# Optimization experiments

Hardware: AMD Instinct MI355X
Metric: run time of the kernel (lower is better)

Reference implementation:

```python
import jax, jax.numpy as jnp
import numpy as np

H = 256; NH = 8; DH = H // NH; L = 2; B = 32; S = 512; FIN = 199; A = 4


def _ln(x, g, b):
    m = jnp.mean(x, -1, keepdims=True)
    v = jnp.mean((x - m) ** 2, -1, keepdims=True)
    return (x - m) / jnp.sqrt(v + 1e-5) * g + b


def _grn(x, fc1w, fc1b, fc2w, fc2b, gw, gb, ggw, ggb, lg, lb):
    # GatedResidualNetwork, input_dim == output_dim so no skip layer, no context
    h = jax.nn.elu(x @ fc1w + fc1b)
    h = jax.nn.elu(h @ fc2w + fc2b)
    g = (h @ gw + gb) * jax.nn.sigmoid(h @ ggw + ggb)  # GLU
    return _ln(g + x, lg, lb)


def _attn(h, wq, bq, wk, bk, wv, bv, wo, bo):
    b, s, _ = h.shape
    q = (h @ wq + bq).reshape(b, s, NH, DH)
    k = (h @ wk + bk).reshape(b, s, NH, DH)
    v = (h @ wv + bv).reshape(b, s, NH, DH)
    scores = jnp.einsum('bqhd,bkhd->bhqk', q, k) / jnp.sqrt(jnp.float32(DH))
    mask = jnp.triu(jnp.ones((s, s), dtype=bool), 1)  # causal: mask strictly-future
    scores = jnp.where(mask, -jnp.inf, scores)
    aw = jax.nn.softmax(scores, axis=-1)
    ctx = jnp.einsum('bhqk,bkhd->bqhd', aw, v).reshape(b, s, H)
    return ctx @ wo + bo, aw


def _pe(s, d):
    pos = jnp.arange(s, dtype=jnp.float32)[:, None]
    div = jnp.exp(jnp.arange(0, d, 2, dtype=jnp.float32) * (-jnp.log(10000.0) / d))
    pe = jnp.zeros((s, d), dtype=jnp.float32)
    pe = pe.at[:, 0::2].set(jnp.sin(pos * div)).at[:, 1::2].set(jnp.cos(pos * div))
    return pe


def setup_inputs():
    key = jax.random.key(0)
    ks = iter(jax.random.split(key, 80))
    def nrm(shape, sc=0.02):
        return (jax.random.normal(next(ks), shape) * sc).astype(jnp.float32)
    d = {}
    d['x'] = jax.random.normal(next(ks), (B, S, FIN), dtype=jnp.float32)
    d['time_features'] = jax.random.normal(next(ks), (B, S, 3), dtype=jnp.float32)
    d['fp_w'] = nrm((FIN, H)); d['fp_b'] = jnp.zeros((H,), jnp.float32)
    d['tp_w'] = nrm((3, H));   d['tp_b'] = jnp.zeros((H,), jnp.float32)
    d['ip_w'] = nrm((H, H));   d['ip_b'] = jnp.zeros((H,), jnp.float32)
    for nm in ['wq', 'wk', 'wv', 'wo']:
        d[nm] = nrm((L, H, H))
    for nm in ['bq', 'bk', 'bv', 'bo']:
        d[nm] = jnp.zeros((L, H), jnp.float32)
    d['ln_g'] = jnp.ones((L, H), jnp.float32); d['ln_b'] = jnp.zeros((L, H), jnp.float32)
    for nm in ['g_fc1w', 'g_fc2w', 'g_gw', 'g_ggw']:
        d[nm] = nrm((L, H, H))
    for nm in ['g_fc1b', 'g_fc2b', 'g_gb', 'g_ggb']:
        d[nm] = jnp.zeros((L, H), jnp.float32)
    d['g_lg'] = jnp.ones((L, H), jnp.float32); d['g_lb'] = jnp.zeros((L, H), jnp.float32)
    for nm in ['f_fc1w', 'f_fc2w', 'f_gw', 'f_ggw']:
        d[nm] = nrm((H, H))
    for nm in ['f_fc1b', 'f_fc2b', 'f_gb', 'f_ggb']:
        d[nm] = jnp.zeros((H,), jnp.float32)
    d['f_lg'] = jnp.ones((H,), jnp.float32); d['f_lb'] = jnp.zeros((H,), jnp.float32)
    d['out_w'] = nrm((H, A)); d['out_b'] = jnp.zeros((A,), jnp.float32)
    return d


def reference(x, time_features, fp_w, fp_b, tp_w, tp_b, ip_w, ip_b,
              wq, bq, wk, bk, wv, bv, wo, bo, ln_g, ln_b,
              g_fc1w, g_fc1b, g_fc2w, g_fc2b, g_gw, g_gb, g_ggw, g_ggb, g_lg, g_lb,
              f_fc1w, f_fc1b, f_fc2w, f_fc2b, f_gw, f_gb, f_ggw, f_ggb, f_lg, f_lb,
              out_w, out_b):
    s = x.shape[1]
    hidden = (x @ fp_w + fp_b) + (time_features @ tp_w + tp_b)
    hidden = hidden @ ip_w + ip_b
    hidden = hidden + _pe(s, H)[None]
    aw = None
    for i in range(L):
        ao, aw = _attn(hidden, wq[i], bq[i], wk[i], bk[i], wv[i], bv[i], wo[i], bo[i])
        hidden = _ln(hidden + ao, ln_g[i], ln_b[i])
        hidden = _grn(hidden, g_fc1w[i], g_fc1b[i], g_fc2w[i], g_fc2b[i],
                      g_gw[i], g_gb[i], g_ggw[i], g_ggb[i], g_lg[i], g_lb[i])
    hidden = _grn(hidden, f_fc1w, f_fc1b, f_fc2w, f_fc2b, f_gw, f_gb, f_ggw, f_ggb, f_lg, f_lb)
    final = hidden[:, -1, :]
    logits = final @ out_w + out_b  # [B, A], one column per target asset
    return (logits, aw)
```

## Files before the change

kernel.cpp:

```cpp
#include <hip/hip_runtime.h>
#include <math.h>
#include <cstddef>

#define H 256
#define NH 8
#define DH 32
#define LAYERS 2
#define BB 32
#define SS 512
#define FINDIM 199
#define AA 4
#define T_TOK (BB*SS)
#define KIN 224

typedef unsigned short u16;
typedef unsigned int u32;
typedef __attribute__((ext_vector_type(8))) short short8;
typedef __attribute__((ext_vector_type(4))) float f4;

__device__ __forceinline__ float b2f(u16 v){
  unsigned u = ((unsigned)v) << 16;
  return __builtin_bit_cast(float, u);
}
__device__ __forceinline__ u16 f2b(float f){
  unsigned u = __builtin_bit_cast(unsigned, f);
  unsigned r = (u + 0x7fffu + ((u >> 16) & 1u)) >> 16;
  return (u16)r;
}
__device__ __forceinline__ float wave_sum(float v){
  #pragma unroll
  for (int mk=1; mk<64; mk<<=1) v += __shfl_xor(v, mk, 64);
  return v;
}

#define GLD_LDS16(g, l) \
  __builtin_amdgcn_global_load_lds((const __attribute__((address_space(1))) void*)(g), \
                                   (__attribute__((address_space(3))) void*)(l), 16, 0, 0)

template<int KC, int WK>
__device__ __forceinline__ void stage_acc(
    const u16* Xl, int sx, const u16* __restrict__ Wt,
    int c0, int l16, int lq, f4 acc[2][2])
{
  #pragma unroll
  for (int mi=0;mi<2;mi++)
    #pragma unroll
    for (int ni=0;ni<2;ni++) acc[mi][ni] = (f4){0.f,0.f,0.f,0.f};
  #pragma unroll
  for (int kc=0;kc<KC;kc++){
    short8 af[2], bf[2];
    af[0] = *(const short8*)&Xl[(l16)*sx      + kc*32 + lq*8];
    af[1] = *(const short8*)&Xl[(16+l16)*sx   + kc*32 + lq*8];
    bf[0] = *(const short8*)(Wt + (size_t)(c0+l16)*WK    + kc*32 + lq*8);
    bf[1] = *(const short8*)(Wt + (size_t)(c0+16+l16)*WK + kc*32 + lq*8);
    #pragma unroll
    for (int mi=0;mi<2;mi++)
      #pragma unroll
      for (int ni=0;ni<2;ni++)
        acc[mi][ni] = __builtin_amdgcn_mfma_f32_16x16x32_bf16(af[mi], bf[ni], acc[mi][ni], 0,0,0);
  }
}

template<int DO_ELU>
__device__ __forceinline__ void stage_store(
    f4 acc[2][2], const float* __restrict__ bias,
    int c0, int l16, int lq, u16* Yl, int sy)
{
  #pragma unroll
  for (int ni=0;ni<2;ni++){
    int col = c0 + ni*16 + l16;
    float bc = bias[col];
    #pragma unroll
    for (int mi=0;mi<2;mi++){
      #pragma unroll
      for (int r=0;r<4;r++){
        int row = mi*16 + lq*4 + r;
        float v = acc[mi][ni][r] + bc;
        if (DO_ELU) v = v > 0.f ? v : expm1f(v);
        Yl[row*sy + col] = f2b(v);
      }
    }
  }
}

__device__ __forceinline__ void tile_load256(const u16* g, u16* Yl, int sy, int t){
  #pragma unroll
  for (int j=0;j<2;j++){
    int u = t + j*512;
    int row = u >> 5, cu = u & 31;
    *(short8*)&Yl[row*sy + cu*8] = *(const short8*)(g + (size_t)row*H + cu*8);
  }
}

__device__ __forceinline__ void tile_ln(
    const u16* Yl, int sy, const float* __restrict__ g, const float* __restrict__ b,
    u16* out, int t)
{
  int w = t >> 6, lane = t & 63;
  #pragma unroll
  for (int rr=0;rr<4;rr++){
    int row = w*4 + rr;
    float xv[4];
    #pragma unroll
    for (int j=0;j<4;j++) xv[j] = b2f(Yl[row*sy + lane*4 + j]);
    float s=0.f, ss=0.f;
    #pragma unroll
    for (int j=0;j<4;j++){ s += xv[j]; ss += xv[j]*xv[j]; }
    s = wave_sum(s); ss = wave_sum(ss);
    float mean = s * (1.0f/H);
    float var  = ss * (1.0f/H) - mean*mean;
    float rstd = rsqrtf(var + 1e-5f);
    ushort4 o;
    int col = lane*4;
    o.x = f2b((xv[0]-mean)*rstd*g[col+0] + b[col+0]);
    o.y = f2b((xv[1]-mean)*rstd*g[col+1] + b[col+1]);
    o.z = f2b((xv[2]-mean)*rstd*g[col+2] + b[col+2]);
    o.w = f2b((xv[3]-mean)*rstd*g[col+3] + b[col+3]);
    *(ushort4*)(out + (size_t)row*H + col) = o;
  }
}

struct WPtrs { const float* p[21]; };

__global__ __launch_bounds__(256) void wconv_kernel(WPtrs wp, u16* __restrict__ dst){
  __shared__ float tl[64][65];
  int mb = blockIdx.x >> 4, tile = blockIdx.x & 15;
  int k0 = (tile >> 2) * 64, n0 = (tile & 3) * 64;
  const float* src = wp.p[mb];
  int t = threadIdx.x;
  int r = t >> 4, cg = t & 15;
  #pragma unroll
  for (int p4=0;p4<4;p4++){
    f4 v = *(const f4*)(src + (size_t)(k0 + r + p4*16)*H + n0 + cg*4);
    tl[r+p4*16][cg*4+0]=v[0]; tl[r+p4*16][cg*4+1]=v[1];
    tl[r+p4*16][cg*4+2]=v[2]; tl[r+p4*16][cg*4+3]=v[3];
  }
  __syncthreads();
  u16* db = dst + (size_t)mb*H*H;
  #pragma unroll
  for (int p4=0;p4<4;p4++){
    int rn = r + p4*16;
    ushort4 o;
    o.x = f2b(tl[cg*4+0][rn]); o.y = f2b(tl[cg*4+1][rn]);
    o.z = f2b(tl[cg*4+2][rn]); o.w = f2b(tl[cg*4+3][rn]);
    *(ushort4*)(db + (size_t)(n0+rn)*H + k0 + cg*4) = o;
  }
}

__global__ __launch_bounds__(256) void wcat_kernel(
    const float* __restrict__ fp_w, const float* __restrict__ tp_w,
    u16* __restrict__ wcat){
  int idx = blockIdx.x*256 + threadIdx.x;
  if (idx >= 256*KIN) return;
  int n = idx / KIN, k2 = idx % KIN;
  float v = 0.f;
  if (k2 < FINDIM) v = fp_w[(size_t)k2*H + n];
  else if (k2 < FINDIM+3) v = tp_w[(size_t)(k2-FINDIM)*H + n];
  wcat[idx] = f2b(v);
}

__global__ __launch_bounds__(256) void xconv_kernel(
    const float* __restrict__ x, const float* __restrict__ tf,
    u16* __restrict__ ab){
  size_t idx = (size_t)blockIdx.x*256 + threadIdx.x;
  if (idx >= (size_t)T_TOK*KIN) return;
  int tok = idx / KIN, k2 = idx % KIN;
  float v = 0.f;
  if (k2 < FINDIM) v = x[(size_t)tok*FINDIM + k2];
  else if (k2 < FINDIM+3) v = tf[(size_t)tok*3 + (k2-FINDIM)];
  ab[idx] = f2b(v);
}

#define SA (KIN+8)
#define SY (H+8)

__global__ __launch_bounds__(512) void input_kernel(
    const u16* __restrict__ ab, const u16* __restrict__ wcat,
    const float* __restrict__ fp_b, const float* __restrict__ tp_b,
    const u16* __restrict__ ipw, const float* __restrict__ ip_b,
    u16* __restrict__ hid){
  __shared__ u16 Al[32*SA];
  __shared__ u16 Tl[32*SY];
  int t = threadIdx.x;
  int tok0 = blockIdx.x * 32;
  int lane = t & 63, w = t >> 6;
  int l16 = lane & 15, lq = lane >> 4;
  int c0 = w * 32;

  #pragma unroll
  for (int j=0;j<2;j++){
    int u = t + j*512;
    if (u < 896){
      int row = u / 28, cu = u % 28;
      *(short8*)&Al[row*SA + cu*8] = *(const short8*)(ab + (size_t)(tok0+row)*KIN + cu*8);
    }
  }
  __syncthreads();

  f4 acc[2][2];
  stage_acc<7, KIN>(Al, SA, wcat, c0, l16, lq, acc);
  #pragma unroll
  for (int ni=0;ni<2;ni++){
    int col = c0 + ni*16 + l16;
    float bc = fp_b[col] + tp_b[col];
    #pragma unroll
    for (int mi=0;mi<2;mi++)
      #pragma unroll
      for (int r=0;r<4;r++){
        int row = mi*16 + lq*4 + r;
        Tl[row*SY + col] = f2b(acc[mi][ni][r] + bc);
      }
  }
  __syncthreads();

  stage_acc<8, H>(Tl, SY, ipw, c0, l16, lq, acc);
  #pragma unroll
  for (int ni=0;ni<2;ni++){
    int col = c0 + ni*16 + l16;
    float bc = ip_b[col];
    int ii = col >> 1;
    float div = __expf((float)(2*ii) * -0.03597789207803197f);
    #pragma unroll
    for (int mi=0;mi<2;mi++)
      #pragma unroll
      for (int r=0;r<4;r++){
        int row = mi*16 + lq*4 + r;
        int s = (tok0 + row) & (SS-1);
        float arg = (float)s * div;
        float pe = (col & 1) ? cosf(arg) : sinf(arg);
        hid[(size_t)(tok0+row)*H + col] = f2b(acc[mi][ni][r] + bc + pe);
      }
  }
}

__global__ __launch_bounds__(512) void oproj_ln_kernel(
    const u16* __restrict__ ctx, u16* __restrict__ hid,
    const u16* __restrict__ wo, const float* __restrict__ bo,
    const float* __restrict__ g, const float* __restrict__ b){
  __shared__ u16 Xl[32*SY];
  __shared__ u16 Rl[32*SY];
  int t = threadIdx.x;
  int tok0 = blockIdx.x * 32;
  int lane = t & 63, w = t >> 6;
  int l16 = lane & 15, lq = lane >> 4;
  int c0 = w * 32;
  u16* hb = hid + (size_t)tok0*H;

  tile_load256(ctx + (size_t)tok0*H, Xl, SY, t);
  tile_load256(hb, Rl, SY, t);
  __syncthreads();

  f4 acc[2][2];
  stage_acc<8, H>(Xl, SY, wo, c0, l16, lq, acc);
  __syncthreads();
  #pragma unroll
  for (int ni=0;ni<2;ni++){
    int col = c0 + ni*16 + l16;
    float bc = bo[col];
    #pragma unroll
    for (int mi=0;mi<2;mi++)
      #pragma unroll
      for (int r=0;r<4;r++){
        int row = mi*16 + lq*4 + r;
        float y = acc[mi][ni][r] + bc + b2f(Rl[row*SY + col]);
        Xl[row*SY + col] = f2b(y);
      }
  }
  __syncthreads();
  tile_ln(Xl, SY, g, b, hb, t);
}

__global__ __launch_bounds__(512) void grn_kernel(
    u16* __restrict__ hid,
    const u16* __restrict__ fc1, const u16* __restrict__ fc2,
    const u16* __restrict__ gw,  const u16* __restrict__ ggw,
    const float* __restrict__ b1, const float* __restrict__ b2,
    const float* __restrict__ gb, const float* __restrict__ ggb,
    const float* __restrict__ lg, const float* __restrict__ lb){
  __shared__ u16 Xl[32*SY];
  __shared__ u16 H1[32*SY];
  __shared__ u16 H2[32*SY];
  int t = threadIdx.x;
  int tok0 = blockIdx.x * 32;
  int lane = t & 63, w = t >> 6;
  int l16 = lane & 15, lq = lane >> 4;
  int c0 = w * 32;
  u16* hb = hid + (size_t)tok0*H;

  tile_load256(hb, Xl, SY, t);
  __syncthreads();

  f4 acc[2][2];
  stage_acc<8, H>(Xl, SY, fc1, c0, l16, lq, acc);
  stage_store<1>(acc, b1, c0, l16, lq, H1, SY);
  __syncthreads();
  stage_acc<8, H>(H1, SY, fc2, c0, l16, lq, acc);
  stage_store<1>(acc, b2, c0, l16, lq, H2, SY);
  __syncthreads();
  stage_acc<8, H>(H2, SY, gw, c0, l16, lq, acc);
  stage_store<0>(acc, gb, c0, l16, lq, H1, SY);
  __syncthreads();
  stage_acc<8, H>(H2, SY, ggw, c0, l16, lq, acc);
  __syncthreads();
  #pragma unroll
  for (int ni=0;ni<2;ni++){
    int col = c0 + ni*16 + l16;
    float bc = ggb[col];
    #pragma unroll
    for (int mi=0;mi<2;mi++)
      #pragma unroll
      for (int r=0;r<4;r++){
        int row = mi*16 + lq*4 + r;
        float gg = acc[mi][ni][r] + bc;
        float sg = 1.0f/(1.0f + __expf(-gg));
        float y  = b2f(H1[row*SY + col]) * sg + b2f(Xl[row*SY + col]);
        H2[row*SY + col] = f2b(y);
      }
  }
  __syncthreads();
  tile_ln(H2, SY, lg, lb, hb, t);
}

struct GemmJob  { const u16* Wt; const float* bias; u16* C; };
struct GemmBatch{ GemmJob j[3]; };

__global__ __launch_bounds__(256) void gemm_bf16(
    const u16* __restrict__ A, GemmBatch jb) {
  __shared__ u16 smem[128*64 + 64*64];
  u16* As  = smem;
  u16* Wsm = smem + 128*64;
  const GemmJob job = jb.j[blockIdx.z];
  const u16* Wt = job.Wt;
  int t = threadIdx.x;
  int m0 = blockIdx.x * 128;
  int n0 = blockIdx.y * 64;
  int lane = t & 63, w = t >> 6;
  int wr = (w >> 1) * 64;
  int wc = (w & 1) * 32;
  int l16 = lane & 15, lq = lane >> 4;

  f4 acc[4][2];
  #pragma unroll
  for (int mi=0;mi<4;mi++)
    #pragma unroll
    for (int ni=0;ni<2;ni++) acc[mi][ni] = (f4){0.f,0.f,0.f,0.f};

  for (int k0=0;k0<256;k0+=64){
    #pragma unroll
    for (int ja=0;ja<4;ja++){
      int ub = (w*4 + ja)*64;
      int u  = ub + lane;
      int m  = u >> 3, c = u & 7, kx = c ^ (m & 7);
      const u16* g = A + (size_t)(m0+m)*H + k0 + kx*8;
      GLD_LDS16(g, As + (size_t)ub*8);
    }
    #pragma unroll
    for (int jb2=0;jb2<2;jb2++){
      int ub = (w*2 + jb2)*64;
      int u  = ub + lane;
      int n  = u >> 3, c = u & 7, kx = c ^ (n & 7);
      const u16* g = Wt + (size_t)(n0+n)*H + k0 + kx*8;
      GLD_LDS16(g, Wsm + (size_t)ub*8);
    }
    __syncthreads();
    #pragma unroll
    for (int kc=0;kc<2;kc++){
      short8 af[4], bf[2];
      int kx = kc*4 + lq;
      #pragma unroll
      for (int mi=0;mi<4;mi++){
        int m = wr + mi*16 + l16;
        int un = (m<<3) | (kx ^ (m&7));
        af[mi] = *(short8*)&As[un*8];
      }
      #pragma unroll
      for (int ni=0;ni<2;ni++){
        int n = wc + ni*16 + l16;
        int un = (n<<3) | (kx ^ (n&7));
        bf[ni] = *(short8*)&Wsm[un*8];
      }
      #pragma unroll
      for (int mi=0;mi<4;mi++)
        #pragma unroll
        for (int ni=0;ni<2;ni++)
          acc[mi][ni] = __builtin_amdgcn_mfma_f32_16x16x32_bf16(af[mi], bf[ni], acc[mi][ni], 0,0,0);
    }
    __syncthreads();
  }

  u16* Cl = smem;
  #pragma unroll
  for (int ni=0;ni<2;ni++){
    int coll = wc + ni*16 + l16;
    float bcol = job.bias[n0 + coll];
    #pragma unroll
    for (int mi=0;mi<4;mi++){
      #pragma unroll
      for (int r=0;r<4;r++){
        int rowl = wr + mi*16 + lq*4 + r;
        Cl[rowl*68 + coll] = f2b(acc[mi][ni][r] + bcol);
      }
    }
  }
  __syncthreads();
  #pragma unroll
  for (int q2=0;q2<4;q2++){
    int u = q2*256 + t;
    int row = u >> 3, cu = u & 7;
    short8 val = *(short8*)&Cl[row*68 + cu*8];
    *(short8*)(job.C + (size_t)(m0+row)*H + n0 + cu*8) = val;
  }
}

template<int WRITE_AW>
__global__ __launch_bounds__(256) void attn_kernel(
    const u16* __restrict__ q, const u16* __restrict__ k,
    const u16* __restrict__ v, float* __restrict__ aw,
    u16* __restrict__ ctx) {
  __shared__ u16 Vt[DH][SS+8];
  __shared__ u16 Plds[4][16][72];
  int t  = threadIdx.x;
  int zg = blockIdx.x;
  int bh = blockIdx.y;
  int b  = bh >> 3, h = bh & 7;
  int lane = t & 63, w = t >> 6;
  int l16 = lane & 15, lq = lane >> 4;
  const float scale = 0.17677669529663687f;

  #pragma unroll
  for (int rep=0;rep<2;rep++){
    int kk = t + rep*256;
    const u16* vp = v + ((size_t)(b*SS + kk))*H + h*DH;
    short8 r0 = *(const short8*)(vp);
    short8 r1 = *(const short8*)(vp+8);
    short8 r2 = *(const short8*)(vp+16);
    short8 r3 = *(const short8*)(vp+24);
    #pragma unroll
    for (int j=0;j<8;j++){
      Vt[j][kk]    = (u16)r0[j];
      Vt[8+j][kk]  = (u16)r1[j];
      Vt[16+j][kk] = (u16)r2[j];
      Vt[24+j][kk] = (u16)r3[j];
    }
  }
  __syncthreads();

  for (int it=0; it<4; it++){
    int qt  = zg + it*2;
    int qr0 = qt*64 + w*16;
    int KT  = qt*4 + w + 1;
    short8 af = *(const short8*)(q + ((size_t)(b*SS + qr0 + l16))*H + h*DH + lq*8);

    float l[4] = {0.f,0.f,0.f,0.f};
    f4 o[2] = {(f4){0.f,0.f,0.f,0.f}, (f4){0.f,0.f,0.f,0.f}};
    u32 pk0[32], pk1[32];

    #pragma unroll
    for (int c8=0;c8<8;c8++){
      if (c8*4 < KT){
        #pragma unroll
        for (int j=0;j<4;j++){
          int kt = c8*4 + j;
          float p[4] = {0.f,0.f,0.f,0.f};
          if (kt < KT){
            short8 bfr = *(const short8*)(k + ((size_t)(b*SS + kt*16 + l16))*H + h*DH + lq*8);
            f4 cc = (f4){0.f,0.f,0.f,0.f};
            cc = __builtin_amdgcn_mfma_f32_16x16x32_bf16(af, bfr, cc, 0,0,0);
            int col = kt*16 + l16;
            #pragma unroll
            for (int i=0;i<4;i++){
              int qi = qr0 + lq*4 + i;
              float sc = (col <= qi) ? cc[i]*scale : -3.0e38f;
              p[i] = __expf(sc);
              l[i] += p[i];
            }
          }
          u16 pb[4];
          #pragma unroll
          for (int i=0;i<4;i++) pb[i] = f2b(p[i]);
          if (WRITE_AW){
            pk0[kt] = (u32)pb[0] | ((u32)pb[1] << 16);
            pk1[kt] = (u32)pb[2] | ((u32)pb[3] << 16);
          }
          #pragma unroll
          for (int i=0;i<4;i++) Plds[w][lq*4+i][j*16+l16] = pb[i];
        }
        #pragma unroll
        for (int kc=0;kc<2;kc++){
          short8 pa = *(short8*)&Plds[w][l16][kc*32 + lq*8];
          #pragma unroll
          for (int dt=0;dt<2;dt++){
            short8 vb = *(const short8*)&Vt[dt*16 + l16][c8*64 + kc*32 + lq*8];
            o[dt] = __builtin_amdgcn_mfma_f32_16x16x32_bf16(pa, vb, o[dt], 0,0,0);
          }
        }
      }
    }

    #pragma unroll
    for (int i=0;i<4;i++){
      #pragma unroll
      for (int mk=1; mk<16; mk<<=1) l[i] += __shfl_xor(l[i], mk, 64);
    }
    float inv[4];
    #pragma unroll
    for (int i=0;i<4;i++) inv[i] = 1.0f / l[i];

    if (WRITE_AW){
      float* ab = aw + (size_t)bh*SS*SS;
      #pragma unroll
      for (int kt=0;kt<32;kt++){
        if (kt < KT){
          int col = kt*16 + l16;
          float pv[4] = { b2f((u16)pk0[kt]), b2f((u16)(pk0[kt]>>16)),
                          b2f((u16)pk1[kt]), b2f((u16)(pk1[kt]>>16)) };
          #pragma unroll
          for (int i=0;i<4;i++){
            int qi = qr0 + lq*4 + i;
            ab[(size_t)qi*SS + col] = (col <= qi) ? pv[i]*inv[i] : 0.f;
          }
        }
      }
      int c4base = KT*4;
      f4 z = (f4){0.f,0.f,0.f,0.f};
      #pragma unroll
      for (int ri=0;ri<4;ri++){
        int row = qr0 + ri*4 + lq;
        for (int j=l16; j < 128 - c4base; j += 16)
          *(f4*)&ab[(size_t)row*SS + (size_t)(c4base+j)*4] = z;
      }
    }

    #pragma unroll
    for (int dt=0;dt<2;dt++){
      #pragma unroll
      for (int i=0;i<4;i++){
        int row = qr0 + lq*4 + i;
        ctx[((size_t)(b*SS + row))*H + h*DH + dt*16 + l16] = f2b(o[dt][i]*inv[i]);
      }
    }
  }
}

__global__ __launch_bounds__(128) void logits_kernel(
    const u16* __restrict__ hid, const float* __restrict__ ow,
    const float* __restrict__ ob, float* __restrict__ out){
  int t = threadIdx.x;
  int b = t >> 2, a = t & 3;
  const u16* hr = hid + ((size_t)b*SS + (SS-1))*H;
  float acc = ob[a];
  for (int k2=0;k2<H;k2++) acc = fmaf(b2f(hr[k2]), ow[k2*AA + a], acc);
  out[t] = acc;
}

extern "C" void kernel_launch(void* const* d_in, const int* in_sizes, int n_in,
                              void* d_out, int out_size, void* d_ws, size_t ws_size,
                              hipStream_t stream){
  (void)in_sizes; (void)n_in; (void)out_size; (void)ws_size;
  const float* x      = (const float*)d_in[0];
  const float* tf     = (const float*)d_in[1];
  const float* fp_w   = (const float*)d_in[2];
  const float* fp_b   = (const float*)d_in[3];
  const float* tp_w   = (const float*)d_in[4];
  const float* tp_b   = (const float*)d_in[5];
  const float* ip_w   = (const float*)d_in[6];
  const float* ip_b   = (const float*)d_in[7];
  const float* wq     = (const float*)d_in[8];
  const float* wk     = (const float*)d_in[9];
  const float* wv     = (const float*)d_in[10];
  const float* wo     = (const float*)d_in[11];
  const float* bq     = (const float*)d_in[12];
  const float* bk     = (const float*)d_in[13];
  const float* bv     = (const float*)d_in[14];
  const float* bo     = (const float*)d_in[15];
  const float* ln_g   = (const float*)d_in[16];
  const float* ln_b   = (const float*)d_in[17];
  const float* g_fc1w = (const float*)d_in[18];
  const float* g_fc2w = (const float*)d_in[19];
  const float* g_gw   = (const float*)d_in[20];
  const float* g_ggw  = (const float*)d_in[21];
  const float* g_fc1b = (const float*)d_in[22];
  const float* g_fc2b = (const float*)d_in[23];
  const float* g_gb   = (const float*)d_in[24];
  const float* g_ggb  = (const float*)d_in[25];
  const float* g_lg   = (const float*)d_in[26];
  const float* g_lb   = (const float*)d_in[27];
  const float* f_fc1w = (const float*)d_in[28];
  const float* f_fc2w = (const float*)d_in[29];
  const float* f_gw   = (const float*)d_in[30];
  const float* f_ggw  = (const float*)d_in[31];
  const float* f_fc1b = (const float*)d_in[32];
  const float* f_fc2b = (const float*)d_in[33];
  const float* f_gb   = (const float*)d_in[34];
  const float* f_ggb  = (const float*)d_in[35];
  const float* f_lg   = (const float*)d_in[36];
  const float* f_lb   = (const float*)d_in[37];
  const float* out_w  = (const float*)d_in[38];
  const float* out_b  = (const float*)d_in[39];

  float* logits = (float*)d_out;
  float* aw     = logits + BB*AA;

  u16* wts = (u16*)d_ws;
  const size_t WMAT = (size_t)H*H;
  u16* wcat = wts  + 21*WMAT;
  u16* abuf = wcat + (size_t)H*KIN;
  u16* hid  = abuf + (size_t)T_TOK*KIN;
  size_t BUF = (size_t)T_TOK * H;
  u16* buf1 = hid  + BUF;
  u16* buf2 = buf1 + BUF;
  u16* buf3 = buf2 + BUF;

  WPtrs wp;
  wp.p[0]  = ip_w;
  wp.p[1]  = wq;        wp.p[2]  = wq + WMAT;
  wp.p[3]  = wk;        wp.p[4]  = wk + WMAT;
  wp.p[5]  = wv;        wp.p[6]  = wv + WMAT;
  wp.p[7]  = wo;        wp.p[8]  = wo + WMAT;
  wp.p[9]  = g_fc1w;    wp.p[10] = g_fc1w + WMAT;
  wp.p[11] = g_fc2w;    wp.p[12] = g_fc2w + WMAT;
  wp.p[13] = g_gw;      wp.p[14] = g_gw + WMAT;
  wp.p[15] = g_ggw;     wp.p[16] = g_ggw + WMAT;
  wp.p[17] = f_fc1w;    wp.p[18] = f_fc2w;
  wp.p[19] = f_gw;      wp.p[20] = f_ggw;
  const int WT_IP=0, WT_Q=1, WT_K=3, WT_V=5, WT_O=7,
            WT_FC1=9, WT_FC2=11, WT_GW=13, WT_GGW=15,
            WT_FFC1=17, WT_FFC2=18, WT_FGW=19, WT_FGGW=20;

  dim3 b256(256), b512(512);
  dim3 gAttn(2, BB*NH);
  dim3 gTok(T_TOK/32);

  wconv_kernel<<<21*16, b256, 0, stream>>>(wp, wts);
  wcat_kernel<<<(H*KIN+255)/256, b256, 0, stream>>>(fp_w, tp_w, wcat);
  xconv_kernel<<<(T_TOK*KIN+255)/256, b256, 0, stream>>>(x, tf, abuf);
  input_kernel<<<gTok, b512, 0, stream>>>(abuf, wcat, fp_b, tp_b,
                                          wts + (size_t)WT_IP*WMAT, ip_b, hid);

  for (int i=0;i<LAYERS;i++){
    const size_t BOFF = (size_t)i*H;
    GemmBatch gb;
    gb.j[0] = { wts + (size_t)(WT_Q+i)*WMAT, bq+BOFF, buf1 };
    gb.j[1] = { wts + (size_t)(WT_K+i)*WMAT, bk+BOFF, buf2 };
    gb.j[2] = { wts + (size_t)(WT_V+i)*WMAT, bv+BOFF, buf3 };
    gemm_bf16<<<dim3(T_TOK/128, H/64, 3), b256, 0, stream>>>(hid, gb);
    if (i == LAYERS-1)
      attn_kernel<1><<<gAttn, b256, 0, stream>>>(buf1, buf2, buf3, aw, buf1);
    else
      attn_kernel<0><<<gAttn, b256, 0, stream>>>(buf1, buf2, buf3, aw, buf1);
    oproj_ln_kernel<<<gTok, b512, 0, stream>>>(buf1, hid,
        wts + (size_t)(WT_O+i)*WMAT, bo+BOFF, ln_g+BOFF, ln_b+BOFF);
    grn_kernel<<<gTok, b512, 0, stream>>>(hid,
        wts + (size_t)(WT_FC1+i)*WMAT, wts + (size_t)(WT_FC2+i)*WMAT,
        wts + (size_t)(WT_GW+i)*WMAT,  wts + (size_t)(WT_GGW+i)*WMAT,
        g_fc1b+BOFF, g_fc2b+BOFF, g_gb+BOFF, g_ggb+BOFF,
        g_lg+BOFF, g_lb+BOFF);
  }

  grn_kernel<<<gTok, b512, 0, stream>>>(hid,
      wts + (size_t)WT_FFC1*WMAT, wts + (size_t)WT_FFC2*WMAT,
      wts + (size_t)WT_FGW*WMAT,  wts + (size_t)WT_FGGW*WMAT,
      f_fc1b, f_fc2b, f_gb, f_ggb, f_lg, f_lb);

  logits_kernel<<<1, 128, 0, stream>>>(hid, out_w, out_b, logits);
}
```

Baseline: 673.6 us.

## Fuse prep kernels, fuse oproj+LN with GRN, coalesce attention-weight stores

Merges the three weight/input conversion kernels into one prep launch. Fuses the output-projection+LayerNorm kernel with the following GRN kernel so the normalized hidden tile stays in LDS instead of round-tripping through global memory. Rewrites the attention-weight write to stage probabilities in LDS and emit float4 row-coalesced stores, and swaps expm1f/sinf/cosf for fast intrinsics. Also adds occupancy hints to launch bounds; fast intrinsics may slightly reduce accuracy, and the new Plds buffer declaration is not visible here.

```diff
diff --git a/kernel.cpp b/kernel.cpp
--- a/kernel.cpp
+++ b/kernel.cpp
@@ -37,6 +37,9 @@
   __builtin_amdgcn_global_load_lds((const __attribute__((address_space(1))) void*)(g), \
                                    (__attribute__((address_space(3))) void*)(l), 16, 0, 0)
 
+#define SA (KIN+8)
+#define SY (H+8)
+
 template<int KC, int WK>
 __device__ __forceinline__ void stage_acc(
     const u16* Xl, int sx, const u16* __restrict__ Wt,
@@ -76,7 +79,7 @@
       for (int r=0;r<4;r++){
         int row = mi*16 + lq*4 + r;
         float v = acc[mi][ni][r] + bc;
-        if (DO_ELU) v = v > 0.f ? v : expm1f(v);
+        if (DO_ELU) v = v > 0.f ? v : (__expf(v) - 1.0f);
         Yl[row*sy + col] = f2b(v);
       }
     }
@@ -92,9 +95,10 @@
   }
 }
 
+template<int TO_LDS>
 __device__ __forceinline__ void tile_ln(
     const u16* Yl, int sy, const float* __restrict__ g, const float* __restrict__ b,
-    u16* out, int t)
+    u16* dst, int t)
 {
   int w = t >> 6, lane = t & 63;
   #pragma unroll
@@ -116,65 +120,61 @@
     o.y = f2b((xv[1]-mean)*rstd*g[col+1] + b[col+1]);
     o.z = f2b((xv[2]-mean)*rstd*g[col+2] + b[col+2]);
     o.w = f2b((xv[3]-mean)*rstd*g[col+3] + b[col+3]);
-    *(ushort4*)(out + (size_t)row*H + col) = o;
+    if (TO_LDS) *(ushort4*)(dst + (size_t)row*SY + col) = o;
+    else        *(ushort4*)(dst + (size_t)row*H  + col) = o;
   }
 }
 
 struct WPtrs { const float* p[21]; };
 
-__global__ __launch_bounds__(256) void wconv_kernel(WPtrs wp, u16* __restrict__ dst){
-  __shared__ float tl[64][65];
-  int mb = blockIdx.x >> 4, tile = blockIdx.x & 15;
-  int k0 = (tile >> 2) * 64, n0 = (tile & 3) * 64;
-  const float* src = wp.p[mb];
+__global__ __launch_bounds__(256) void prep_kernel(
+    WPtrs wp, u16* __restrict__ wts,
+    const float* __restrict__ fp_w, const float* __restrict__ tp_w,
+    u16* __restrict__ wcat,
+    const float* __restrict__ x, const float* __restrict__ tf,
+    u16* __restrict__ abuf){
+  int bid = blockIdx.x;
   int t = threadIdx.x;
-  int r = t >> 4, cg = t & 15;
-  #pragma unroll
-  for (int p4=0;p4<4;p4++){
-    f4 v = *(const f4*)(src + (size_t)(k0 + r + p4*16)*H + n0 + cg*4);
-    tl[r+p4*16][cg*4+0]=v[0]; tl[r+p4*16][cg*4+1]=v[1];
-    tl[r+p4*16][cg*4+2]=v[2]; tl[r+p4*16][cg*4+3]=v[3];
-  }
-  __syncthreads();
-  u16* db = dst + (size_t)mb*H*H;
-  #pragma unroll
-  for (int p4=0;p4<4;p4++){
-    int rn = r + p4*16;
-    ushort4 o;
-    o.x = f2b(tl[cg*4+0][rn]); o.y = f2b(tl[cg*4+1][rn]);
-    o.z = f2b(tl[cg*4+2][rn]); o.w = f2b(tl[cg*4+3][rn]);
-    *(ushort4*)(db + (size_t)(n0+rn)*H + k0 + cg*4) = o;
-  }
-}
-
-__global__ __launch_bounds__(256) void wcat_kernel(
-    const float* __restrict__ fp_w, const float* __restrict__ tp_w,
-    u16* __restrict__ wcat){
-  int idx = blockIdx.x*256 + threadIdx.x;
-  if (idx >= 256*KIN) return;
-  int n = idx / KIN, k2 = idx % KIN;
-  float v = 0.f;
-  if (k2 < FINDIM) v = fp_w[(size_t)k2*H + n];
-  else if (k2 < FINDIM+3) v = tp_w[(size_t)(k2-FINDIM)*H + n];
-  wcat[idx] = f2b(v);
-}
-
-__global__ __launch_bounds__(256) void xconv_kernel(
-    const float* __restrict__ x, const float* __restrict__ tf,
-    u16* __restrict__ ab){
-  size_t idx = (size_t)blockIdx.x*256 + threadIdx.x;
-  if (idx >= (size_t)T_TOK*KIN) return;
-  int tok = idx / KIN, k2 = idx % KIN;
-  float v = 0.f;
-  if (k2 < FINDIM) v = x[(size_t)tok*FINDIM + k2];
-  else if (k2 < FINDIM+3) v = tf[(size_t)tok*3 + (k2-FINDIM)];
-  ab[idx] = f2b(v);
-}
-
-#define SA (KIN+8)
-#define SY (H+8)
-
-__global__ __launch_bounds__(512) void input_kernel(
+  if (bid < 336){
+    __shared__ float tl[64][65];
+    int mb = bid >> 4, tile = bid & 15;
+    int k0 = (tile >> 2) * 64, n0 = (tile & 3) * 64;
+    const float* src = wp.p[mb];
+    int r = t >> 4, cg = t & 15;
+    #pragma unroll
+    for (int p4=0;p4<4;p4++){
+      f4 v = *(const f4*)(src + (size_t)(k0 + r + p4*16)*H + n0 + cg*4);
+      tl[r+p4*16][cg*4+0]=v[0]; tl[r+p4*16][cg*4+1]=v[1];
+      tl[r+p4*16][cg*4+2]=v[2]; tl[r+p4*16][cg*4+3]=v[3];
+    }
+    __syncthreads();
+    u16* db = wts + (size_t)mb*H*H;
+    #pragma unroll
+    for (int p4=0;p4<4;p4++){
+      int rn = r + p4*16;
+      ushort4 o;
+      o.x = f2b(tl[cg*4+0][rn]); o.y = f2b(tl[cg*4+1][rn]);
+      o.z = f2b(tl[cg*4+2][rn]); o.w = f2b(tl[cg*4+3][rn]);
+      *(ushort4*)(db + (size_t)(n0+rn)*H + k0 + cg*4) = o;
+    }
+  } else if (bid < 336+224){
+    int idx = (bid-336)*256 + t;
+    int n = idx / KIN, k2 = idx % KIN;
+    float v = 0.f;
+    if (k2 < FINDIM) v = fp_w[(size_t)k2*H + n];
+    else if (k2 < FINDIM+3) v = tp_w[(size_t)(k2-FINDIM)*H + n];
+    wcat[idx] = f2b(v);
+  } else {
+    size_t idx = (size_t)(bid-560)*256 + t;
+    int tok = idx / KIN, k2 = idx % KIN;
+    float v = 0.f;
+    if (k2 < FINDIM) v = x[(size_t)tok*FINDIM + k2];
+    else if (k2 < FINDIM+3) v = tf[(size_t)tok*3 + (k2-FINDIM)];
+    abuf[idx] = f2b(v);
+  }
+}
+
+__global__ __launch_bounds__(512, 4) void input_kernel(
     const u16* __restrict__ ab, const u16* __restrict__ wcat,
     const float* __restrict__ fp_b, const float* __restrict__ tp_b,
     const u16* __restrict__ ipw, const float* __restrict__ ip_b,
@@ -227,80 +227,69 @@
         int row = mi*16 + lq*4 + r;
         int s = (tok0 + row) & (SS-1);
         float arg = (float)s * div;
-        float pe = (col & 1) ? cosf(arg) : sinf(arg);
+        float pe = (col & 1) ? __cosf(arg) : __sinf(arg);
         hid[(size_t)(tok0+row)*H + col] = f2b(acc[mi][ni][r] + bc + pe);
       }
   }
 }
 
-__global__ __launch_bounds__(512) void oproj_ln_kernel(
+template<int WITH_OPROJ>
+__global__ __launch_bounds__(512, 4) void post_kernel(
     const u16* __restrict__ ctx, u16* __restrict__ hid,
     const u16* __restrict__ wo, const float* __restrict__ bo,
-    const float* __restrict__ g, const float* __restrict__ b){
+    const float* __restrict__ lng, const float* __restrict__ lnb,
+    const u16* __restrict__ fc1, const u16* __restrict__ fc2,
+    const u16* __restrict__ gw,  const u16* __restrict__ ggw,
+    const float* __restrict__ b1, const float* __restrict__ b2,
+    const float* __restrict__ gb, const float* __restrict__ ggb,
+    const float* __restrict__ lg, const float* __restrict__ lb){
   __shared__ u16 Xl[32*SY];
   __shared__ u16 Rl[32*SY];
+  __shared__ u16 H1[32*SY];
   int t = threadIdx.x;
   int tok0 = blockIdx.x * 32;
   int lane = t & 63, w = t >> 6;
   int l16 = lane & 15, lq = lane >> 4;
   int c0 = w * 32;
   u16* hb = hid + (size_t)tok0*H;
-
-  tile_load256(ctx + (size_t)tok0*H, Xl, SY, t);
-  tile_load256(hb, Rl, SY, t);
-  __syncthreads();
-
   f4 acc[2][2];
-  stage_acc<8, H>(Xl, SY, wo, c0, l16, lq, acc);
-  __syncthreads();
-  #pragma unroll
-  for (int ni=0;ni<2;ni++){
-    int col = c0 + ni*16 + l16;
-    float bc = bo[col];
-    #pragma unroll
-    for (int mi=0;mi<2;mi++)
-      #pragma unroll
-      for (int r=0;r<4;r++){
-        int row = mi*16 + lq*4 + r;
-        float y = acc[mi][ni][r] + bc + b2f(Rl[row*SY + col]);
-        Xl[row*SY + col] = f2b(y);
-      }
-  }
-  __syncthreads();
-  tile_ln(Xl, SY, g, b, hb, t);
-}
-
-__global__ __launch_bounds__(512) void grn_kernel(
-    u16* __restrict__ hid,
-    const u16* __restrict__ fc1, const u16* __restrict__ fc2,
-    const u16* __restrict__ gw,  const u16* __restrict__ ggw,
-    const float* __restrict__ b1, const float* __restrict__ b2,
-    const float* __restrict__ gb, const float* __restrict__ ggb,
-    const float* __restrict__ lg, const float* __restrict__ lb){
-  __shared__ u16 Xl[32*SY];
-  __shared__ u16 H1[32*SY];
-  __shared__ u16 H2[32*SY];
-  int t = threadIdx.x;
-  int tok0 = blockIdx.x * 32;
-  int lane = t & 63, w = t >> 6;
-  int l16 = lane & 15, lq = lane >> 4;
-  int c0 = w * 32;
-  u16* hb = hid + (size_t)tok0*H;
-
-  tile_load256(hb, Xl, SY, t);
-  __syncthreads();
-
-  f4 acc[2][2];
-  stage_acc<8, H>(Xl, SY, fc1, c0, l16, lq, acc);
-  stage_store<1>(acc, b1, c0, l16, lq, H1, SY);
-  __syncthreads();
-  stage_acc<8, H>(H1, SY, fc2, c0, l16, lq, acc);
-  stage_store<1>(acc, b2, c0, l16, lq, H2, SY);
-  __syncthreads();
-  stage_acc<8, H>(H2, SY, gw, c0, l16, lq, acc);
-  stage_store<0>(acc, gb, c0, l16, lq, H1, SY);
-  __syncthreads();
-  stage_acc<8, H>(H2, SY, ggw, c0, l16, lq, acc);
+
+  if (WITH_OPROJ){
+    tile_load256(ctx + (size_t)tok0*H, Xl, SY, t);
+    tile_load256(hb, Rl, SY, t);
+    __syncthreads();
+    stage_acc<8, H>(Xl, SY, wo, c0, l16, lq, acc);
+    __syncthreads();
+    #pragma unroll
+    for (int ni=0;ni<2;ni++){
+      int col = c0 + ni*16 + l16;
+      float bc = bo[col];
+      #pragma unroll
+      for (int mi=0;mi<2;mi++)
+        #pragma unroll
+        for (int r=0;r<4;r++){
+          int row = mi*16 + lq*4 + r;
+          Xl[row*SY + col] = f2b(acc[mi][ni][r] + bc + b2f(Rl[row*SY + col]));
+        }
+    }
+    __syncthreads();
+    tile_ln<1>(Xl, SY, lng, lnb, Rl, t);
+    __syncthreads();
+  } else {
+    tile_load256(hb, Rl, SY, t);
+    __syncthreads();
+  }
+
+  stage_acc<8, H>(Rl, SY, fc1, c0, l16, lq, acc);
+  stage_store<1>(acc, b1, c0, l16, lq, Xl, SY);
+  __syncthreads();
+  stage_acc<8, H>(Xl, SY, fc2, c0, l16, lq, acc);
+  stage_store<1>(acc, b2, c0, l16, lq, H1, SY);
+  __syncthreads();
+  stage_acc<8, H>(H1, SY, gw, c0, l16, lq, acc);
+  stage_store<0>(acc, gb, c0, l16, lq, Xl, SY);
+  __syncthreads();
+  stage_acc<8, H>(H1, SY, ggw, c0, l16, lq, acc);
   __syncthreads();
   #pragma unroll
   for (int ni=0;ni<2;ni++){
@@ -313,12 +302,12 @@
         int row = mi*16 + lq*4 + r;
         float gg = acc[mi][ni][r] + bc;
         float sg = 1.0f/(1.0f + __expf(-gg));
-        float y  = b2f(H1[row*SY + col]) * sg + b2f(Xl[row*SY + col]);
-        H2[row*SY + col] = f2b(y);
-      }
-  }
-  __syncthreads();
-  tile_ln(H2, SY, lg, lb, hb, t);
+        float y  = b2f(Xl[row*SY + col]) * sg + b2f(Rl[row*SY + col]);
+        H1[row*SY + col] = f2b(y);
+      }
+  }
+  __syncthreads();
+  tile_ln<0>(H1, SY, lg, lb, hb, t);
 }
 
 struct GemmJob  { const u16* Wt; const float* bias; u16* C; };
@@ -509,25 +498,38 @@
     if (WRITE_AW){
       float* ab = aw + (size_t)bh*SS*SS;
       #pragma unroll
-      for (int kt=0;kt<32;kt++){
-        if (kt < KT){
-          int col = kt*16 + l16;
-          float pv[4] = { b2f((u16)pk0[kt]), b2f((u16)(pk0[kt]>>16)),
-                          b2f((u16)pk1[kt]), b2f((u16)(pk1[kt]>>16)) };
+      for (int c8=0;c8<8;c8++){
+        int cbase = c8*64;
+        if (c8*4 < KT){
           #pragma unroll
-          for (int i=0;i<4;i++){
-            int qi = qr0 + lq*4 + i;
-            ab[(size_t)qi*SS + col] = (col <= qi) ? pv[i]*inv[i] : 0.f;
+          for (int j=0;j<4;j++){
+            int kt = c8*4 + j;
+            float pv[4] = {0.f,0.f,0.f,0.f};
+            if (kt < KT){
+              pv[0]=b2f((u16)pk0[kt]); pv[1]=b2f((u16)(pk0[kt]>>16));
+              pv[2]=b2f((u16)pk1[kt]); pv[3]=b2f((u16)(pk1[kt]>>16));
+            }
+            #pragma unroll
+            for (int i=0;i<4;i++) Plds[w][lq*4+i][j*16+l16] = f2b(pv[i]*inv[i]);
+          }
+          #pragma unroll
+          for (int r4=0;r4<4;r4++){
+            int row = r4*4 + lq;
+            float4 o4;
+            o4.x = b2f(Plds[w][row][l16*4+0]);
+            o4.y = b2f(Plds[w][row][l16*4+1]);
+            o4.z = b2f(Plds[w][row][l16*4+2]);
+            o4.w = b2f(Plds[w][row][l16*4+3]);
+            *(float4*)&ab[(size_t)(qr0+row)*SS + cbase + l16*4] = o4;
+          }
+        } else {
+          f4 z = (f4){0.f,0.f,0.f,0.f};
+          #pragma unroll
+          for (int r4=0;r4<4;r4++){
+            int row = r4*4 + lq;
+            *(f4*)&ab[(size_t)(qr0+row)*SS + cbase + l16*4] = z;
           }
         }
-      }
-      int c4base = KT*4;
-      f4 z = (f4){0.f,0.f,0.f,0.f};
-      #pragma unroll
-      for (int ri=0;ri<4;ri++){
-        int row = qr0 + ri*4 + lq;
-        for (int j=l16; j < 128 - c4base; j += 16)
-          *(f4*)&ab[(size_t)row*SS + (size_t)(c4base+j)*4] = z;
       }
     }
 
@@ -631,9 +633,7 @@
   dim3 gAttn(2, BB*NH);
   dim3 gTok(T_TOK/32);
 
-  wconv_kernel<<<21*16, b256, 0, stream>>>(wp, wts);
-  wcat_kernel<<<(H*KIN+255)/256, b256, 0, stream>>>(fp_w, tp_w, wcat);
-  xconv_kernel<<<(T_TOK*KIN+255)/256, b256, 0, stream>>>(x, tf, abuf);
+  prep_kernel<<<336+224+14336, b256, 0, stream>>>(wp, wts, fp_w, tp_w, wcat, x, tf, abuf);
   input_kernel<<<gTok, b512, 0, stream>>>(abuf, wcat, fp_b, tp_b,
                                           wts + (size_t)WT_IP*WMAT, ip_b, hid);
 
@@ -648,16 +648,16 @@
       attn_kernel<1><<<gAttn, b256, 0, stream>>>(buf1, buf2, buf3, aw, buf1);
     else
       attn_kernel<0><<<gAttn, b256, 0, stream>>>(buf1, buf2, buf3, aw, buf1);
-    oproj_ln_kernel<<<gTok, b512, 0, stream>>>(buf1, hid,
-        wts + (size_t)(WT_O+i)*WMAT, bo+BOFF, ln_g+BOFF, ln_b+BOFF);
-    grn_kernel<<<gTok, b512, 0, stream>>>(hid,
+    post_kernel<1><<<gTok, b512, 0, stream>>>(buf1, hid,
+        wts + (size_t)(WT_O+i)*WMAT, bo+BOFF, ln_g+BOFF, ln_b+BOFF,
         wts + (size_t)(WT_FC1+i)*WMAT, wts + (size_t)(WT_FC2+i)*WMAT,
         wts + (size_t)(WT_GW+i)*WMAT,  wts + (size_t)(WT_GGW+i)*WMAT,
         g_fc1b+BOFF, g_fc2b+BOFF, g_gb+BOFF, g_ggb+BOFF,
         g_lg+BOFF, g_lb+BOFF);
   }
 
-  grn_kernel<<<gTok, b512, 0, stream>>>(hid,
+  post_kernel<0><<<gTok, b512, 0, stream>>>(nullptr, hid,
+      nullptr, nullptr, nullptr, nullptr,
       wts + (size_t)WT_FFC1*WMAT, wts + (size_t)WT_FFC2*WMAT,
       wts + (size_t)WT_FGW*WMAT,  wts + (size_t)WT_FGGW*WMAT,
       f_fc1b, f_fc2b, f_gb, f_ggb, f_lg, f_lb);
```

Result: no change. 683.5 us (+1.5%).
